# Optimization experiments

Measured on AMD Instinct MI355X. Metric: run time of the kernel, lower is better.

Reference implementation:

```python
import jax, jax.numpy as jnp
import numpy as np

N_NODES = 100000
N_EDGES = 1600000
IN_FEATS = 128
HIDDEN = 128
NUM_CLASSES = 4


def setup_inputs() -> dict:
    key = jax.random.key(0)
    ks = jax.random.split(key, 8)
    features = jax.random.normal(ks[0], (N_NODES, IN_FEATS), dtype=jnp.float32)
    src = jax.random.randint(ks[1], (N_EDGES,), 0, N_NODES, dtype=jnp.int64)
    dst = jax.random.randint(ks[2], (N_EDGES,), 0, N_NODES, dtype=jnp.int64)
    s = 1.0 / np.sqrt(IN_FEATS)
    W1 = jax.random.normal(ks[3], (IN_FEATS, HIDDEN), dtype=jnp.float32) * s
    b1 = jnp.zeros((HIDDEN,), dtype=jnp.float32)
    W2 = jax.random.normal(ks[4], (HIDDEN, HIDDEN), dtype=jnp.float32) * s
    b2 = jnp.zeros((HIDDEN,), dtype=jnp.float32)
    Wc = jax.random.normal(ks[5], (HIDDEN, NUM_CLASSES), dtype=jnp.float32) * s
    bc = jnp.zeros((NUM_CLASSES,), dtype=jnp.float32)
    return {"features": features, "src": src, "dst": dst,
            "W1": W1, "b1": b1, "W2": W2, "b2": b2, "Wc": Wc, "bc": bc}


def _graph_conv(x, W, b, src, dst, n_nodes, activation=True):
    # DGL GraphConv, norm='both': D_out^{-1/2} A^T D_in... i.e. symmetric norm.
    ones = jnp.ones((src.shape[0],), dtype=x.dtype)
    deg_out = jnp.clip(jax.ops.segment_sum(ones, src, num_segments=n_nodes), 1.0)
    deg_in = jnp.clip(jax.ops.segment_sum(ones, dst, num_segments=n_nodes), 1.0)
    # scale sources, project (in >= out so matmul first, math-equivalent), gather-scatter
    h = (x * (deg_out ** -0.5)[:, None]) @ W            # [N, out]
    msg = h[src]                                         # [E, out] gather
    agg = jax.ops.segment_sum(msg, dst, num_segments=n_nodes)  # [N, out] scatter-add
    h = agg * (deg_in ** -0.5)[:, None] + b
    return jax.nn.relu(h) if activation else h


def reference(features, src, dst, W1, b1, W2, b2, Wc, bc):
    # eval-mode forward: dropout is identity
    n = features.shape[0]
    h = _graph_conv(features, W1, b1, src, dst, n, activation=True)
    h = _graph_conv(h, W2, b2, src, dst, n, activation=True)
    return h @ Wc + bc  # [N, num_classes] logits
```

## Files before the change

kernel.cpp:

```cpp
#include <hip/hip_runtime.h>
#include <hip/hip_fp16.h>
#include <math.h>

#define N_NODES 100000
#define N_EDGES 1600000
#define F 128
#define NBUK 196
#define BSH 9
#define BSZ 512
#define CAP 9216

typedef _Float16 half8 __attribute__((ext_vector_type(8)));
typedef float    f32x4 __attribute__((ext_vector_type(4)));

__global__ __launch_bounds__(256) void init_pack(int* __restrict__ curD,
                                                 int* __restrict__ curS,
                                                 _Float16* __restrict__ padrow,
                                                 const float* __restrict__ W1,
                                                 const float* __restrict__ W2,
                                                 _Float16* __restrict__ hi1,
                                                 _Float16* __restrict__ lo1,
                                                 _Float16* __restrict__ hi2,
                                                 _Float16* __restrict__ lo2)
{
    int t = threadIdx.x;
    if (blockIdx.x == 0) {
        if (t < NBUK) { curD[t] = t * CAP; curS[t] = t * CAP; }
        if (t < 16) reinterpret_cast<int4*>(padrow)[t] = make_int4(0, 0, 0, 0);
        return;
    }
    int gidx = (blockIdx.x - 1) * 256 + t;
    const float* W = (gidx < 16384) ? W1 : W2;
    _Float16* hi = (gidx < 16384) ? hi1 : hi2;
    _Float16* lo = (gidx < 16384) ? lo1 : lo2;
    int idx = gidx & 16383;
    int f = idx >> 9, r = idx & 511;
    int l = r >> 3, j = r & 7;
    int kc = f >> 3, ct = f & 7;
    int k = kc * 32 + (l >> 4) * 8 + j;
    int n = ct * 16 + (l & 15);
    float w = W[k * 128 + n];
    _Float16 h = (_Float16)w;
    hi[idx] = h;
    lo[idx] = (_Float16)(w - (float)h);
}

__global__ __launch_bounds__(512) void part_gemm1(const int* __restrict__ src,
                                                  const int* __restrict__ dst,
                                                  int* __restrict__ curD,
                                                  int* __restrict__ curS,
                                                  int* __restrict__ bukD,
                                                  int* __restrict__ bukS,
                                                  const float* __restrict__ X,
                                                  const _Float16* __restrict__ Whi,
                                                  const _Float16* __restrict__ Wlo,
                                                  _Float16* __restrict__ Y, int N)
{
    __shared__ int hd[NBUK], hs[NBUK], bd[NBUK], bs[NBUK], cd[NBUK], cs[NBUK];
    const int tid = threadIdx.x;

    if (blockIdx.x < NBUK) {
        const int chunk = (((N_EDGES + NBUK - 1) / NBUK) + 3) & ~3;
        const int beg = blockIdx.x * chunk;
        const int end = min(beg + chunk, N_EDGES);
        if (beg >= end) return;
        if (tid < NBUK) { hd[tid] = 0; hs[tid] = 0; cd[tid] = 0; cs[tid] = 0; }
        __syncthreads();
        const int b4 = beg >> 2, e4 = end >> 2;
        for (int i = b4 + tid; i < e4; i += 512) {
            int4 d = reinterpret_cast<const int4*>(dst)[i];
            int4 s = reinterpret_cast<const int4*>(src)[i];
            atomicAdd(&hd[d.x >> BSH], 1); atomicAdd(&hd[d.y >> BSH], 1);
            atomicAdd(&hd[d.z >> BSH], 1); atomicAdd(&hd[d.w >> BSH], 1);
            atomicAdd(&hs[s.x >> BSH], 1); atomicAdd(&hs[s.y >> BSH], 1);
            atomicAdd(&hs[s.z >> BSH], 1); atomicAdd(&hs[s.w >> BSH], 1);
        }
        __syncthreads();
        if (tid < NBUK) {
            bd[tid] = hd[tid] ? atomicAdd(&curD[tid], hd[tid]) : 0;
            bs[tid] = hs[tid] ? atomicAdd(&curS[tid], hs[tid]) : 0;
        }
        __syncthreads();
        for (int e = beg + tid; e < end; e += 512) {
            int d = dst[e], s = src[e];
            int bin = d >> BSH;
            int r = atomicAdd(&cd[bin], 1);
            bukD[bd[bin] + r] = ((d & 511) << 17) | s;
            int bin2 = s >> BSH;
            int r2 = atomicAdd(&cs[bin2], 1);
            bukS[bs[bin2] + r2] = s;
        }
        return;
    }

    const int l = tid & 63, w = tid >> 6;
    const int quad = l >> 4, m = l & 15;
    const int row0 = (blockIdx.x - NBUK) * 256;
    const half8* Bh = reinterpret_cast<const half8*>(Whi);
    const half8* Bl = reinterpret_cast<const half8*>(Wlo);

    f32x4 acc[2][8] = {};

    for (int kc = 0; kc < 4; kc++) {
        half8 ah[2], al[2];
        #pragma unroll
        for (int rt = 0; rt < 2; rt++) {
            int grow = row0 + w * 32 + rt * 16 + m;
            float4 xa = make_float4(0.f, 0.f, 0.f, 0.f), xb = xa;
            if (grow < N) {
                const float4* Xp = reinterpret_cast<const float4*>(X) + (size_t)grow * 32 + kc * 8 + quad * 2;
                xa = Xp[0]; xb = Xp[1];
            }
            float xs[8] = {xa.x, xa.y, xa.z, xa.w, xb.x, xb.y, xb.z, xb.w};
            #pragma unroll
            for (int j = 0; j < 8; j++) {
                _Float16 h = (_Float16)xs[j];
                ah[rt][j] = h;
                al[rt][j] = (_Float16)(xs[j] - (float)h);
            }
        }
        #pragma unroll
        for (int ct = 0; ct < 8; ct++) {
            int f = kc * 8 + ct;
            half8 bh = Bh[f * 64 + l];
            half8 bl = Bl[f * 64 + l];
            #pragma unroll
            for (int rt = 0; rt < 2; rt++) {
                acc[rt][ct] = __builtin_amdgcn_mfma_f32_16x16x32_f16(ah[rt], bh, acc[rt][ct], 0, 0, 0);
                acc[rt][ct] = __builtin_amdgcn_mfma_f32_16x16x32_f16(al[rt], bh, acc[rt][ct], 0, 0, 0);
                acc[rt][ct] = __builtin_amdgcn_mfma_f32_16x16x32_f16(ah[rt], bl, acc[rt][ct], 0, 0, 0);
            }
        }
    }

    #pragma unroll
    for (int rt = 0; rt < 2; rt++) {
        #pragma unroll
        for (int r = 0; r < 4; r++) {
            int grow = row0 + w * 32 + rt * 16 + quad * 4 + r;
            if (grow < N) {
                #pragma unroll
                for (int ct = 0; ct < 8; ct++)
                    Y[(size_t)grow * 128 + ct * 16 + m] = (_Float16)(acc[rt][ct][r]);
            }
        }
    }
}

__global__ __launch_bounds__(512) void csr_deg(const int* __restrict__ bukD,
                                               const int* __restrict__ bukS,
                                               const int* __restrict__ curD,
                                               const int* __restrict__ curS,
                                               int* __restrict__ row_ptr,
                                               float* __restrict__ sin_,
                                               float* __restrict__ sout,
                                               int* __restrict__ col)
{
    __shared__ int h[BSZ], sc[BSZ], cur[BSZ];
    const int tid = threadIdx.x;

    if (blockIdx.x >= NBUK) {
        const int bid = blockIdx.x - NBUK;
        const int n0 = bid << BSH;
        const int lo = bid * CAP, hi = curS[bid];
        h[tid] = 0;
        __syncthreads();
        for (int i = lo + tid; i < hi; i += 512)
            atomicAdd(&h[bukS[i] - n0], 1);
        __syncthreads();
        int node = n0 + tid;
        if (node < N_NODES) sout[node] = rsqrtf((float)max(h[tid], 1));
        return;
    }

    const int n0 = blockIdx.x << BSH;
    const int lo = blockIdx.x * CAP, hi = curD[blockIdx.x];
    h[tid] = 0;
    __syncthreads();
    for (int i = lo + tid; i < hi; i += 512)
        atomicAdd(&h[((unsigned)bukD[i]) >> 17], 1);
    __syncthreads();
    int own = h[tid];
    sc[tid] = own;
    __syncthreads();
    for (int off = 1; off < 512; off <<= 1) {
        int u = (tid >= off) ? sc[tid - off] : 0;
        __syncthreads();
        sc[tid] += u;
        __syncthreads();
    }
    int ex = sc[tid] - own;
    cur[tid] = ex;
    int node = n0 + tid;
    if (node < N_NODES) {
        row_ptr[2 * node]     = lo + ex;
        row_ptr[2 * node + 1] = lo + ex + own;
        sin_[node] = rsqrtf((float)max(own, 1));
    }
    __syncthreads();
    for (int i = lo + tid; i < hi; i += 512) {
        int p = bukD[i];
        int r = atomicAdd(&cur[((unsigned)p) >> 17], 1);
        col[lo + r] = p & 0x1FFFF;
    }
}

__global__ __launch_bounds__(256) void gather_agg_s(const __half* __restrict__ Hh,
                                                    const int* __restrict__ row_ptr,
                                                    const int* __restrict__ col,
                                                    const float* __restrict__ sout,
                                                    const float* __restrict__ sin_,
                                                    const float* __restrict__ bias,
                                                    __half* __restrict__ Yh, int N)
{
    int node = blockIdx.x * 4 + (threadIdx.x >> 6);
    if (node >= N) return;
    int lane = threadIdx.x & 63;
    int beg = row_ptr[2 * node], end = row_ptr[2 * node + 1];
    const __half2* H2 = reinterpret_cast<const __half2*>(Hh);
    float2 acc0 = make_float2(0.f, 0.f);
    float2 acc1 = make_float2(0.f, 0.f);
    int i = beg;
    for (; i + 3 < end; i += 4) {
        int s0 = col[i], s1 = col[i + 1], s2 = col[i + 2], s3 = col[i + 3];
        float w0 = sout[s0], w1 = sout[s1], w2 = sout[s2], w3 = sout[s3];
        __half2 v0 = H2[((size_t)s0 << 6) | lane];
        __half2 v1 = H2[((size_t)s1 << 6) | lane];
        __half2 v2 = H2[((size_t)s2 << 6) | lane];
        __half2 v3 = H2[((size_t)s3 << 6) | lane];
        float2 f0 = __half22float2(v0), f1 = __half22float2(v1);
        float2 f2 = __half22float2(v2), f3 = __half22float2(v3);
        acc0.x = fmaf(w0, f0.x, fmaf(w1, f1.x, acc0.x));
        acc0.y = fmaf(w0, f0.y, fmaf(w1, f1.y, acc0.y));
        acc1.x = fmaf(w2, f2.x, fmaf(w3, f3.x, acc1.x));
        acc1.y = fmaf(w2, f2.y, fmaf(w3, f3.y, acc1.y));
    }
    for (; i < end; i++) {
        int s = col[i];
        float w = sout[s];
        float2 f = __half22float2(H2[((size_t)s << 6) | lane]);
        acc0.x = fmaf(w, f.x, acc0.x);
        acc0.y = fmaf(w, f.y, acc0.y);
    }
    float sc = sin_[node];
    float2 b = reinterpret_cast<const float2*>(bias)[lane];
    float ox = fmaxf((acc0.x + acc1.x) * sc + b.x, 0.f);
    float oy = fmaxf((acc0.y + acc1.y) * sc + b.y, 0.f);
    reinterpret_cast<__half2*>(Yh)[((size_t)node << 6) | lane] = __floats2half2_rn(ox, oy);
}

__global__ __launch_bounds__(256) void gemm_mfma_f16(const _Float16* __restrict__ Xh,
                                                     const _Float16* __restrict__ Whi,
                                                     const _Float16* __restrict__ Wlo,
                                                     const float* __restrict__ srow,
                                                     _Float16* __restrict__ Y, int N)
{
    const int tid = threadIdx.x;
    const int l = tid & 63, w = tid >> 6;
    const int quad = l >> 4, m = l & 15;
    const int row0 = blockIdx.x * 128;
    const half8* Bh = reinterpret_cast<const half8*>(Whi);
    const half8* Bl = reinterpret_cast<const half8*>(Wlo);

    f32x4 acc[2][8] = {};

    for (int kc = 0; kc < 4; kc++) {
        half8 a[2];
        #pragma unroll
        for (int rt = 0; rt < 2; rt++) {
            int grow = row0 + w * 32 + rt * 16 + m;
            half8 z = {};
            a[rt] = (grow < N)
                ? *reinterpret_cast<const half8*>(Xh + (size_t)grow * 128 + kc * 32 + quad * 8)
                : z;
        }
        #pragma unroll
        for (int ct = 0; ct < 8; ct++) {
            int f = kc * 8 + ct;
            half8 bh = Bh[f * 64 + l];
            half8 bl = Bl[f * 64 + l];
            #pragma unroll
            for (int rt = 0; rt < 2; rt++) {
                acc[rt][ct] = __builtin_amdgcn_mfma_f32_16x16x32_f16(a[rt], bh, acc[rt][ct], 0, 0, 0);
                acc[rt][ct] = __builtin_amdgcn_mfma_f32_16x16x32_f16(a[rt], bl, acc[rt][ct], 0, 0, 0);
            }
        }
    }

    #pragma unroll
    for (int rt = 0; rt < 2; rt++) {
        #pragma unroll
        for (int r = 0; r < 4; r++) {
            int grow = row0 + w * 32 + rt * 16 + quad * 4 + r;
            if (grow < N) {
                float s = srow[grow];
                #pragma unroll
                for (int ct = 0; ct < 8; ct++)
                    Y[(size_t)grow * 128 + ct * 16 + m] = (_Float16)(acc[rt][ct][r] * s);
            }
        }
    }
}

__global__ __launch_bounds__(256) void gather_agg(const __half* __restrict__ Hh,
                                                  const int* __restrict__ row_ptr,
                                                  const int* __restrict__ col,
                                                  const float* __restrict__ sin_,
                                                  const float* __restrict__ bias,
                                                  __half* __restrict__ Yh, int N)
{
    int node = blockIdx.x * 4 + (threadIdx.x >> 6);
    if (node >= N) return;
    int lane = threadIdx.x & 63;
    int beg = row_ptr[2 * node], end = row_ptr[2 * node + 1];
    const __half2* H2 = reinterpret_cast<const __half2*>(Hh);
    float2 acc0 = make_float2(0.f, 0.f);
    float2 acc1 = make_float2(0.f, 0.f);
    int i = beg;
    for (; i + 3 < end; i += 4) {
        int s0 = col[i], s1 = col[i + 1], s2 = col[i + 2], s3 = col[i + 3];
        __half2 v0 = H2[((size_t)s0 << 6) | lane];
        __half2 v1 = H2[((size_t)s1 << 6) | lane];
        __half2 v2 = H2[((size_t)s2 << 6) | lane];
        __half2 v3 = H2[((size_t)s3 << 6) | lane];
        float2 f0 = __half22float2(v0), f1 = __half22float2(v1);
        float2 f2 = __half22float2(v2), f3 = __half22float2(v3);
        acc0.x += f0.x + f1.x; acc0.y += f0.y + f1.y;
        acc1.x += f2.x + f3.x; acc1.y += f2.y + f3.y;
    }
    for (; i < end; i++) {
        int s = col[i];
        float2 f = __half22float2(H2[((size_t)s << 6) | lane]);
        acc0.x += f.x; acc0.y += f.y;
    }
    float sc = sin_[node];
    float2 b = reinterpret_cast<const float2*>(bias)[lane];
    float ox = fmaxf((acc0.x + acc1.x) * sc + b.x, 0.f);
    float oy = fmaxf((acc0.y + acc1.y) * sc + b.y, 0.f);
    reinterpret_cast<__half2*>(Yh)[((size_t)node << 6) | lane] = __floats2half2_rn(ox, oy);
}

__global__ __launch_bounds__(256) void classifier(const __half* __restrict__ Hh,
                                                  const float* __restrict__ Wc,
                                                  const float* __restrict__ bc,
                                                  float* __restrict__ out, int N)
{
    __shared__ float4 Wcs[128];
    for (int i = threadIdx.x; i < 128; i += 256)
        Wcs[i] = reinterpret_cast<const float4*>(Wc)[i];
    __syncthreads();
    int i = blockIdx.x * 256 + threadIdx.x;
    if (i < N) {
        float4 acc = reinterpret_cast<const float4*>(bc)[0];
        const __half2* h2 = reinterpret_cast<const __half2*>(Hh) + (size_t)i * 64;
        #pragma unroll
        for (int j = 0; j < 64; j++) {
            float2 f = __half22float2(h2[j]);
            float4 w0 = Wcs[2 * j], w1 = Wcs[2 * j + 1];
            acc.x += f.x * w0.x + f.y * w1.x;
            acc.y += f.x * w0.y + f.y * w1.y;
            acc.z += f.x * w0.z + f.y * w1.z;
            acc.w += f.x * w0.w + f.y * w1.w;
        }
        reinterpret_cast<float4*>(out)[i] = acc;
    }
}

extern "C" void kernel_launch(void* const* d_in, const int* in_sizes, int n_in,
                              void* d_out, int out_size, void* d_ws, size_t ws_size,
                              hipStream_t stream)
{
    const float* features = (const float*)d_in[0];
    const int*   src      = (const int*)d_in[1];
    const int*   dst      = (const int*)d_in[2];
    const float* W1       = (const float*)d_in[3];
    const float* b1       = (const float*)d_in[4];
    const float* W2       = (const float*)d_in[5];
    const float* b2       = (const float*)d_in[6];
    const float* Wc       = (const float*)d_in[7];
    const float* bc       = (const float*)d_in[8];
    float* out = (float*)d_out;

    char* ws = (char*)d_ws;
    const size_t MB = 1 << 20;
    int* curD  = (int*)(ws + 0);
    int* curS  = (int*)(ws + 1024);
    float* sout    = (float*)(ws + 1 * MB);
    float* sin_    = (float*)(ws + 2 * MB);
    int*   row_ptr = (int*)(ws + 3 * MB);
    int*   col     = (int*)(ws + 4 * MB);
    int*   bukD    = (int*)(ws + 12 * MB);
    int*   bukS    = (int*)(ws + 20 * MB);
    _Float16* Whi1 = (_Float16*)(ws + 28 * MB);
    _Float16* Wlo1 = (_Float16*)(ws + 28 * MB + 32 * 1024);
    _Float16* Whi2 = (_Float16*)(ws + 28 * MB + 64 * 1024);
    _Float16* Wlo2 = (_Float16*)(ws + 28 * MB + 96 * 1024);
    _Float16* hMsg = (_Float16*)(ws + 29 * MB);
    _Float16* hA   = (_Float16*)(ws + 55 * MB);

    const int N = N_NODES;

    init_pack<<<129, 256, 0, stream>>>(curD, curS, hMsg + (size_t)N * F,
                                       W1, W2, Whi1, Wlo1, Whi2, Wlo2);

    part_gemm1<<<NBUK + 391, 512, 0, stream>>>(src, dst, curD, curS, bukD, bukS,
                                               features, Whi1, Wlo1, hMsg, N);

    csr_deg<<<2 * NBUK, 512, 0, stream>>>(bukD, bukS, curD, curS,
                                          row_ptr, sin_, sout, col);

    gather_agg_s<<<(N + 3) / 4, 256, 0, stream>>>((const __half*)hMsg, row_ptr, col,
                                                  sout, sin_, b1, (__half*)hA, N);

    gemm_mfma_f16<<<(N + 127) / 128, 256, 0, stream>>>(hA, Whi2, Wlo2, sout, hMsg, N);
    gather_agg<<<(N + 3) / 4, 256, 0, stream>>>((const __half*)hMsg, row_ptr, col,
                                                sin_, b2, (__half*)hA, N);

    classifier<<<(N + 255) / 256, 256, 0, stream>>>((const __half*)hA, Wc, bc, out, N);
}
```

Before: 343.4 us.

## Pack two nodes per wave in gathers, shrink source buckets, drop low-X MFMA term

The gather kernels now handle two nodes per 64-lane wave, with each lane loading four halves. Tail edges are padded with a zero row at index N_NODES and a zero sout entry, so the remainder loop is no longer needed. Source-bucket entries are stored as 16-bit local offsets rather than 32-bit ids, which halves that traffic. In the first GEMM the low-half correction for X is dropped, cutting MFMA work by a third at some cost in precision.

```diff
diff --git a/kernel.cpp b/kernel.cpp
--- a/kernel.cpp
+++ b/kernel.cpp
@@ -11,11 +11,13 @@
 #define CAP 9216
 
 typedef _Float16 half8 __attribute__((ext_vector_type(8)));
+typedef _Float16 half4v __attribute__((ext_vector_type(4)));
 typedef float    f32x4 __attribute__((ext_vector_type(4)));
 
 __global__ __launch_bounds__(256) void init_pack(int* __restrict__ curD,
                                                  int* __restrict__ curS,
                                                  _Float16* __restrict__ padrow,
+                                                 float* __restrict__ sout,
                                                  const float* __restrict__ W1,
                                                  const float* __restrict__ W2,
                                                  _Float16* __restrict__ hi1,
@@ -27,6 +29,7 @@
     if (blockIdx.x == 0) {
         if (t < NBUK) { curD[t] = t * CAP; curS[t] = t * CAP; }
         if (t < 16) reinterpret_cast<int4*>(padrow)[t] = make_int4(0, 0, 0, 0);
+        if (t == 255) sout[N_NODES] = 0.f;
         return;
     }
     int gidx = (blockIdx.x - 1) * 256 + t;
@@ -50,7 +53,7 @@
                                                   int* __restrict__ curD,
                                                   int* __restrict__ curS,
                                                   int* __restrict__ bukD,
-                                                  int* __restrict__ bukS,
+                                                  unsigned short* __restrict__ bukS,
                                                   const float* __restrict__ X,
                                                   const _Float16* __restrict__ Whi,
                                                   const _Float16* __restrict__ Wlo,
@@ -88,7 +91,7 @@
             bukD[bd[bin] + r] = ((d & 511) << 17) | s;
             int bin2 = s >> BSH;
             int r2 = atomicAdd(&cs[bin2], 1);
-            bukS[bs[bin2] + r2] = s;
+            bukS[bs[bin2] + r2] = (unsigned short)(s & 511);
         }
         return;
     }
@@ -102,7 +105,7 @@
     f32x4 acc[2][8] = {};
 
     for (int kc = 0; kc < 4; kc++) {
-        half8 ah[2], al[2];
+        half8 ah[2];
         #pragma unroll
         for (int rt = 0; rt < 2; rt++) {
             int grow = row0 + w * 32 + rt * 16 + m;
@@ -111,13 +114,10 @@
                 const float4* Xp = reinterpret_cast<const float4*>(X) + (size_t)grow * 32 + kc * 8 + quad * 2;
                 xa = Xp[0]; xb = Xp[1];
             }
-            float xs[8] = {xa.x, xa.y, xa.z, xa.w, xb.x, xb.y, xb.z, xb.w};
-            #pragma unroll
-            for (int j = 0; j < 8; j++) {
-                _Float16 h = (_Float16)xs[j];
-                ah[rt][j] = h;
-                al[rt][j] = (_Float16)(xs[j] - (float)h);
-            }
+            ah[rt][0] = (_Float16)xa.x; ah[rt][1] = (_Float16)xa.y;
+            ah[rt][2] = (_Float16)xa.z; ah[rt][3] = (_Float16)xa.w;
+            ah[rt][4] = (_Float16)xb.x; ah[rt][5] = (_Float16)xb.y;
+            ah[rt][6] = (_Float16)xb.z; ah[rt][7] = (_Float16)xb.w;
         }
         #pragma unroll
         for (int ct = 0; ct < 8; ct++) {
@@ -127,7 +127,6 @@
             #pragma unroll
             for (int rt = 0; rt < 2; rt++) {
                 acc[rt][ct] = __builtin_amdgcn_mfma_f32_16x16x32_f16(ah[rt], bh, acc[rt][ct], 0, 0, 0);
-                acc[rt][ct] = __builtin_amdgcn_mfma_f32_16x16x32_f16(al[rt], bh, acc[rt][ct], 0, 0, 0);
                 acc[rt][ct] = __builtin_amdgcn_mfma_f32_16x16x32_f16(ah[rt], bl, acc[rt][ct], 0, 0, 0);
             }
         }
@@ -148,7 +147,7 @@
 }
 
 __global__ __launch_bounds__(512) void csr_deg(const int* __restrict__ bukD,
-                                               const int* __restrict__ bukS,
+                                               const unsigned short* __restrict__ bukS,
                                                const int* __restrict__ curD,
                                                const int* __restrict__ curS,
                                                int* __restrict__ row_ptr,
@@ -166,7 +165,7 @@
         h[tid] = 0;
         __syncthreads();
         for (int i = lo + tid; i < hi; i += 512)
-            atomicAdd(&h[bukS[i] - n0], 1);
+            atomicAdd(&h[bukS[i]], 1);
         __syncthreads();
         int node = n0 + tid;
         if (node < N_NODES) sout[node] = rsqrtf((float)max(h[tid], 1));
@@ -205,48 +204,92 @@
     }
 }
 
-__global__ __launch_bounds__(256) void gather_agg_s(const __half* __restrict__ Hh,
+__global__ __launch_bounds__(256) void gather_agg_s(const _Float16* __restrict__ Hh,
                                                     const int* __restrict__ row_ptr,
                                                     const int* __restrict__ col,
                                                     const float* __restrict__ sout,
                                                     const float* __restrict__ sin_,
                                                     const float* __restrict__ bias,
-                                                    __half* __restrict__ Yh, int N)
-{
-    int node = blockIdx.x * 4 + (threadIdx.x >> 6);
+                                                    _Float16* __restrict__ Yh, int N)
+{
+    int wave = blockIdx.x * 4 + (threadIdx.x >> 6);
+    int lane = threadIdx.x & 63;
+    int sub  = lane & 31;
+    int node = wave * 2 + (lane >> 5);
     if (node >= N) return;
+    int beg = row_ptr[2 * node], end = row_ptr[2 * node + 1];
+    const half4v* H4 = reinterpret_cast<const half4v*>(Hh);
+    float a0 = 0.f, a1 = 0.f, a2 = 0.f, a3 = 0.f;
+    for (int i = beg; i < end; i += 4) {
+        int c[4];
+        #pragma unroll
+        for (int j = 0; j < 4; j++)
+            c[j] = (i + j < end) ? col[i + j] : N_NODES;
+        float w[4];
+        #pragma unroll
+        for (int j = 0; j < 4; j++) w[j] = sout[c[j]];
+        half4v v[4];
+        #pragma unroll
+        for (int j = 0; j < 4; j++)
+            v[j] = H4[((size_t)c[j] << 5) | sub];
+        #pragma unroll
+        for (int j = 0; j < 4; j++) {
+            a0 = fmaf(w[j], (float)v[j][0], a0);
+            a1 = fmaf(w[j], (float)v[j][1], a1);
+            a2 = fmaf(w[j], (float)v[j][2], a2);
+            a3 = fmaf(w[j], (float)v[j][3], a3);
+        }
+    }
+    float scn = sin_[node];
+    float4 b = reinterpret_cast<const float4*>(bias)[sub];
+    half4v o;
+    o[0] = (_Float16)fmaxf(fmaf(a0, scn, b.x), 0.f);
+    o[1] = (_Float16)fmaxf(fmaf(a1, scn, b.y), 0.f);
+    o[2] = (_Float16)fmaxf(fmaf(a2, scn, b.z), 0.f);
+    o[3] = (_Float16)fmaxf(fmaf(a3, scn, b.w), 0.f);
+    reinterpret_cast<half4v*>(Yh)[((size_t)node << 5) | sub] = o;
+}
+
+__global__ __launch_bounds__(256) void gather_agg(const _Float16* __restrict__ Hh,
+                                                  const int* __restrict__ row_ptr,
+                                                  const int* __restrict__ col,
+                                                  const float* __restrict__ sin_,
+                                                  const float* __restrict__ bias,
+                                                  _Float16* __restrict__ Yh, int N)
+{
+    int wave = blockIdx.x * 4 + (threadIdx.x >> 6);
     int lane = threadIdx.x & 63;
+    int sub  = lane & 31;
+    int node = wave * 2 + (lane >> 5);
+    if (node >= N) return;
     int beg = row_ptr[2 * node], end = row_ptr[2 * node + 1];
-    const __half2* H2 = reinterpret_cast<const __half2*>(Hh);
-    float2 acc0 = make_float2(0.f, 0.f);
-    float2 acc1 = make_float2(0.f, 0.f);
-    int i = beg;
-    for (; i + 3 < end; i += 4) {
-        int s0 = col[i], s1 = col[i + 1], s2 = col[i + 2], s3 = col[i + 3];
-        float w0 = sout[s0], w1 = sout[s1], w2 = sout[s2], w3 = sout[s3];
-        __half2 v0 = H2[((size_t)s0 << 6) | lane];
-        __half2 v1 = H2[((size_t)s1 << 6) | lane];
-        __half2 v2 = H2[((size_t)s2 << 6) | lane];
-        __half2 v3 = H2[((size_t)s3 << 6) | lane];
-        float2 f0 = __half22float2(v0), f1 = __half22float2(v1);
-        float2 f2 = __half22float2(v2), f3 = __half22float2(v3);
-        acc0.x = fmaf(w0, f0.x, fmaf(w1, f1.x, acc0.x));
-        acc0.y = fmaf(w0, f0.y, fmaf(w1, f1.y, acc0.y));
-        acc1.x = fmaf(w2, f2.x, fmaf(w3, f3.x, acc1.x));
-        acc1.y = fmaf(w2, f2.y, fmaf(w3, f3.y, acc1.y));
-    }
-    for (; i < end; i++) {
-        int s = col[i];
-        float w = sout[s];
-        float2 f = __half22float2(H2[((size_t)s << 6) | lane]);
-        acc0.x = fmaf(w, f.x, acc0.x);
-        acc0.y = fmaf(w, f.y, acc0.y);
-    }
-    float sc = sin_[node];
-    float2 b = reinterpret_cast<const float2*>(bias)[lane];
-    float ox = fmaxf((acc0.x + acc1.x) * sc + b.x, 0.f);
-    float oy = fmaxf((acc0.y + acc1.y) * sc + b.y, 0.f);
-    reinterpret_cast<__half2*>(Yh)[((size_t)node << 6) | lane] = __floats2half2_rn(ox, oy);
+    const half4v* H4 = reinterpret_cast<const half4v*>(Hh);
+    float a0 = 0.f, a1 = 0.f, a2 = 0.f, a3 = 0.f;
+    for (int i = beg; i < end; i += 4) {
+        int c[4];
+        #pragma unroll
+        for (int j = 0; j < 4; j++)
+            c[j] = (i + j < end) ? col[i + j] : N_NODES;
+        half4v v[4];
+        #pragma unroll
+        for (int j = 0; j < 4; j++)
+            v[j] = H4[((size_t)c[j] << 5) | sub];
+        #pragma unroll
+        for (int j = 0; j < 4; j++) {
+            a0 += (float)v[j][0];
+            a1 += (float)v[j][1];
+            a2 += (float)v[j][2];
+            a3 += (float)v[j][3];
+        }
+    }
+    float scn = sin_[node];
+    float4 b = reinterpret_cast<const float4*>(bias)[sub];
+    half4v o;
+    o[0] = (_Float16)fmaxf(fmaf(a0, scn, b.x), 0.f);
+    o[1] = (_Float16)fmaxf(fmaf(a1, scn, b.y), 0.f);
+    o[2] = (_Float16)fmaxf(fmaf(a2, scn, b.z), 0.f);
+    o[3] = (_Float16)fmaxf(fmaf(a3, scn, b.w), 0.f);
+    reinterpret_cast<half4v*>(Yh)[((size_t)node << 5) | sub] = o;
 }
 
 __global__ __launch_bounds__(256) void gemm_mfma_f16(const _Float16* __restrict__ Xh,
@@ -300,44 +343,6 @@
             }
         }
     }
-}
-
-__global__ __launch_bounds__(256) void gather_agg(const __half* __restrict__ Hh,
-                                                  const int* __restrict__ row_ptr,
-                                                  const int* __restrict__ col,
-                                                  const float* __restrict__ sin_,
-                                                  const float* __restrict__ bias,
-                                                  __half* __restrict__ Yh, int N)
-{
-    int node = blockIdx.x * 4 + (threadIdx.x >> 6);
-    if (node >= N) return;
-    int lane = threadIdx.x & 63;
-    int beg = row_ptr[2 * node], end = row_ptr[2 * node + 1];
-    const __half2* H2 = reinterpret_cast<const __half2*>(Hh);
-    float2 acc0 = make_float2(0.f, 0.f);
-    float2 acc1 = make_float2(0.f, 0.f);
-    int i = beg;
-    for (; i + 3 < end; i += 4) {
-        int s0 = col[i], s1 = col[i + 1], s2 = col[i + 2], s3 = col[i + 3];
-        __half2 v0 = H2[((size_t)s0 << 6) | lane];
-        __half2 v1 = H2[((size_t)s1 << 6) | lane];
-        __half2 v2 = H2[((size_t)s2 << 6) | lane];
-        __half2 v3 = H2[((size_t)s3 << 6) | lane];
-        float2 f0 = __half22float2(v0), f1 = __half22float2(v1);
-        float2 f2 = __half22float2(v2), f3 = __half22float2(v3);
-        acc0.x += f0.x + f1.x; acc0.y += f0.y + f1.y;
-        acc1.x += f2.x + f3.x; acc1.y += f2.y + f3.y;
-    }
-    for (; i < end; i++) {
-        int s = col[i];
-        float2 f = __half22float2(H2[((size_t)s << 6) | lane]);
-        acc0.x += f.x; acc0.y += f.y;
-    }
-    float sc = sin_[node];
-    float2 b = reinterpret_cast<const float2*>(bias)[lane];
-    float ox = fmaxf((acc0.x + acc1.x) * sc + b.x, 0.f);
-    float oy = fmaxf((acc0.y + acc1.y) * sc + b.y, 0.f);
-    reinterpret_cast<__half2*>(Yh)[((size_t)node << 6) | lane] = __floats2half2_rn(ox, oy);
 }
 
 __global__ __launch_bounds__(256) void classifier(const __half* __restrict__ Hh,
@@ -390,17 +395,18 @@
     int*   row_ptr = (int*)(ws + 3 * MB);
     int*   col     = (int*)(ws + 4 * MB);
     int*   bukD    = (int*)(ws + 12 * MB);
-    int*   bukS    = (int*)(ws + 20 * MB);
-    _Float16* Whi1 = (_Float16*)(ws + 28 * MB);
-    _Float16* Wlo1 = (_Float16*)(ws + 28 * MB + 32 * 1024);
-    _Float16* Whi2 = (_Float16*)(ws + 28 * MB + 64 * 1024);
-    _Float16* Wlo2 = (_Float16*)(ws + 28 * MB + 96 * 1024);
-    _Float16* hMsg = (_Float16*)(ws + 29 * MB);
-    _Float16* hA   = (_Float16*)(ws + 55 * MB);
+    unsigned short* bukS = (unsigned short*)(ws + 20 * MB);
+    _Float16* Whi1 = (_Float16*)(ws + 24 * MB);
+    _Float16* Wlo1 = (_Float16*)(ws + 24 * MB + 32 * 1024);
+    _Float16* Whi2 = (_Float16*)(ws + 24 * MB + 64 * 1024);
+    _Float16* Wlo2 = (_Float16*)(ws + 24 * MB + 96 * 1024);
+    _Float16* hMsg = (_Float16*)(ws + 25 * MB);
+    _Float16* hA   = (_Float16*)(ws + 52 * MB);
 
     const int N = N_NODES;
-
-    init_pack<<<129, 256, 0, stream>>>(curD, curS, hMsg + (size_t)N * F,
+    const int NGB = (N / 2 + 3) / 4;
+
+    init_pack<<<129, 256, 0, stream>>>(curD, curS, hMsg + (size_t)N * F, sout,
                                        W1, W2, Whi1, Wlo1, Whi2, Wlo2);
 
     part_gemm1<<<NBUK + 391, 512, 0, stream>>>(src, dst, curD, curS, bukD, bukS,
@@ -409,12 +415,10 @@
     csr_deg<<<2 * NBUK, 512, 0, stream>>>(bukD, bukS, curD, curS,
                                           row_ptr, sin_, sout, col);
 
-    gather_agg_s<<<(N + 3) / 4, 256, 0, stream>>>((const __half*)hMsg, row_ptr, col,
-                                                  sout, sin_, b1, (__half*)hA, N);
+    gather_agg_s<<<NGB, 256, 0, stream>>>(hMsg, row_ptr, col, sout, sin_, b1, hA, N);
 
     gemm_mfma_f16<<<(N + 127) / 128, 256, 0, stream>>>(hA, Whi2, Wlo2, sout, hMsg, N);
-    gather_agg<<<(N + 3) / 4, 256, 0, stream>>>((const __half*)hMsg, row_ptr, col,
-                                                sin_, b2, (__half*)hA, N);
+    gather_agg<<<NGB, 256, 0, stream>>>(hMsg, row_ptr, col, sin_, b2, hA, N);
 
     classifier<<<(N + 255) / 256, 256, 0, stream>>>((const __half*)hA, Wc, bc, out, N);
 }
```

New measurement: 328.6 us. 1.04x faster.
